# Kernel tuning notes

Hardware: AMD Instinct MI355X
Metric: run time of the kernel (lower is better)

The kernel has to match this reference:

```python
import jax, jax.numpy as jnp
import numpy as np

# Grouped TF->gene sparse decoder dims
T = 512       # number of TFs (tf_size)
K = 4         # nodes_per_tf (width_multiplier); decoder_features = T*K = 2048
G = 20000     # number of genes (gene_size)
EPG = 3       # regulating TFs per gene (TF-gene edges per gene)
B = 512       # batch of cells


def setup_inputs() -> dict:
    key = jax.random.key(0)
    k0, k1, k2, k3, k4, k5, k6 = jax.random.split(key, 7)
    features = jax.random.normal(k0, (B, T), dtype=jnp.float32)
    # Layer 1: each TF fans out to its own K hidden nodes (one weight per edge)
    w1 = jax.random.normal(k1, (T, K), dtype=jnp.float32) * 0.5
    b1 = jax.random.normal(k2, (T, K), dtype=jnp.float32) * 0.1
    # Layer 2: block-dense KxK mixing within each TF group
    w2 = jax.random.normal(k3, (T, K, K), dtype=jnp.float32) * (1.0 / np.sqrt(K))
    b2 = jax.random.normal(k4, (T, K), dtype=jnp.float32) * 0.1
    # Output layer: gene g sums over its EPG TF edges x K hidden nodes
    w3 = jax.random.normal(k5, (G, EPG, K), dtype=jnp.float32) * (1.0 / np.sqrt(EPG * K))
    b3 = jax.random.normal(k6, (G,), dtype=jnp.float32) * 0.1
    # Fixed irregular TF-gene connectivity (constant structure, like data_obj)
    edge_tf = jnp.asarray(
        np.random.default_rng(0).integers(0, T, size=(G, EPG)), dtype=jnp.int32
    )
    return {"features": features, "w1": w1, "b1": b1, "w2": w2, "b2": b2,
            "w3": w3, "b3": b3, "edge_tf": edge_tf}


def reference(features, w1, b1, w2, b2, w3, b3, edge_tf):
    # SparseLinear decoder_1: TF t -> its K hidden nodes, then LeakyReLU(0.01)
    h1 = jax.nn.leaky_relu(features[:, :, None] * w1 + b1)            # [B,T,K]
    # SparseLinear decoder_2: block-dense within each TF group + LeakyReLU
    h2 = jax.nn.leaky_relu(jnp.einsum('btj,tjk->btk', h1, w2) + b2)   # [B,T,K]
    # SparseLinear output: gather each gene's regulating TF groups, contract
    gathered = h2[:, edge_tf, :]                                      # [B,G,EPG,K]
    out = jnp.einsum('bgek,gek->bg', gathered, w3) + b3               # [B,G]
    return out
```

## Files before the change

kernel.cpp:

```cpp
#include <hip/hip_runtime.h>

namespace {

constexpr int T = 512;
constexpr int K = 4;
constexpr int G = 20000;
constexpr int EPG = 3;
constexpr int B = 512;
constexpr float SLOPE = 0.01f;

__device__ __forceinline__ float lrelu(float x) { return x > 0.0f ? x : SLOPE * x; }

__global__ __launch_bounds__(256) void h2_kernel(
    const float* __restrict__ features, const float* __restrict__ w1,
    const float* __restrict__ b1, const float* __restrict__ w2,
    const float* __restrict__ b2, float* __restrict__ h2out) {
  const int t = blockIdx.x * 256 + threadIdx.x;
  const int b = blockIdx.y;
  const float f = features[b * T + t];
  const float4 W1 = reinterpret_cast<const float4*>(w1)[t];
  const float4 B1 = reinterpret_cast<const float4*>(b1)[t];
  const float4 B2 = reinterpret_cast<const float4*>(b2)[t];
  const float h0 = lrelu(f * W1.x + B1.x);
  const float h1 = lrelu(f * W1.y + B1.y);
  const float h2 = lrelu(f * W1.z + B1.z);
  const float h3 = lrelu(f * W1.w + B1.w);
  const float4* W2 = reinterpret_cast<const float4*>(w2 + (size_t)t * (K * K));
  const float4 r0 = W2[0];
  const float4 r1 = W2[1];
  const float4 r2 = W2[2];
  const float4 r3 = W2[3];
  float4 o;
  o.x = lrelu(B2.x + h0 * r0.x + h1 * r1.x + h2 * r2.x + h3 * r3.x);
  o.y = lrelu(B2.y + h0 * r0.y + h1 * r1.y + h2 * r2.y + h3 * r3.y);
  o.z = lrelu(B2.z + h0 * r0.z + h1 * r1.z + h2 * r2.z + h3 * r3.z);
  o.w = lrelu(B2.w + h0 * r0.w + h1 * r1.w + h2 * r2.w + h3 * r3.w);
  reinterpret_cast<float4*>(h2out)[b * T + t] = o;
}

constexpr int GPT = 4;
constexpr int BTILE = 16;

__global__ __launch_bounds__(256) void out_kernel(
    const float* __restrict__ h2, const float* __restrict__ w3,
    const float* __restrict__ b3, const int* __restrict__ edge,
    float* __restrict__ out) {
  __shared__ float4 row[2][T];
  const int tid = threadIdx.x;
  const int gbase = blockIdx.x * (GPT * 256);
  const int b0 = blockIdx.y * BTILE;

  int gg[GPT];
  int te[GPT][EPG];
  float4 w3v[GPT][EPG];
  float bias[GPT];
  bool valid[GPT];
#pragma unroll
  for (int i = 0; i < GPT; ++i) {
    const int g = gbase + i * 256 + tid;
    gg[i] = g;
    valid[i] = (g < G);
    if (valid[i]) {
#pragma unroll
      for (int e = 0; e < EPG; ++e) te[i][e] = edge[g * EPG + e];
      const float4* wp = reinterpret_cast<const float4*>(w3 + (size_t)g * (EPG * K));
      w3v[i][0] = wp[0];
      w3v[i][1] = wp[1];
      w3v[i][2] = wp[2];
      bias[i] = b3[g];
    } else {
#pragma unroll
      for (int e = 0; e < EPG; ++e) te[i][e] = 0;
      w3v[i][0] = w3v[i][1] = w3v[i][2] = make_float4(0.f, 0.f, 0.f, 0.f);
      bias[i] = 0.f;
    }
  }

  {
    const float4* src = reinterpret_cast<const float4*>(h2 + (size_t)b0 * T * K);
    row[0][tid] = src[tid];
    row[0][tid + 256] = src[tid + 256];
  }

  for (int ib = 0; ib < BTILE; ++ib) {
    const int cur = ib & 1;
    __syncthreads();
    if (ib + 1 < BTILE) {
      const float4* src =
          reinterpret_cast<const float4*>(h2 + (size_t)(b0 + ib + 1) * T * K);
      row[cur ^ 1][tid] = src[tid];
      row[cur ^ 1][tid + 256] = src[tid + 256];
    }
    const int b = b0 + ib;
#pragma unroll
    for (int i = 0; i < GPT; ++i) {
      if (!valid[i]) continue;
      float acc = bias[i];
#pragma unroll
      for (int e = 0; e < EPG; ++e) {
        const float4 v = row[cur][te[i][e]];
        const float4 w = w3v[i][e];
        acc += v.x * w.x + v.y * w.y + v.z * w.z + v.w * w.w;
      }
      out[(size_t)b * G + gg[i]] = acc;
    }
  }
}

}

extern "C" void kernel_launch(void* const* d_in, const int* in_sizes, int n_in,
                              void* d_out, int out_size, void* d_ws, size_t ws_size,
                              hipStream_t stream) {
  const float* features = (const float*)d_in[0];
  const float* w1 = (const float*)d_in[1];
  const float* b1 = (const float*)d_in[2];
  const float* w2 = (const float*)d_in[3];
  const float* b2 = (const float*)d_in[4];
  const float* w3 = (const float*)d_in[5];
  const float* b3 = (const float*)d_in[6];
  const int* edge = (const int*)d_in[7];
  float* out = (float*)d_out;
  float* h2buf = (float*)d_ws;

  dim3 g1(T / 256, B);
  h2_kernel<<<g1, 256, 0, stream>>>(features, w1, b1, w2, b2, h2buf);

  dim3 g2((G + GPT * 256 - 1) / (GPT * 256), B / BTILE);
  out_kernel<<<g2, 256, 0, stream>>>(h2buf, w3, b3, edge, out);
}
```

Before: 101.4 us.

## Pack per-gene weights into records and transpose h2 tile in LDS by batch

Adds a prep kernel that packs each gene's w3 weights, bias and pre-scaled LDS byte offsets for its TFs into a 64-byte record. The output kernel loads an 8-batch tile of h2 into LDS transposed as [T][8 batches x K] with padded stride, so 8 lanes read adjacent batches of the same TF. It loops over genes with software-prefetched records. This is meant to cut per-thread register state and improve gather locality, at the cost of an extra kernel launch and rereading records for every batch tile. Output stores become strided across batches within a wave.

```diff
diff --git a/kernel.cpp b/kernel.cpp
--- a/kernel.cpp
+++ b/kernel.cpp
@@ -7,6 +7,9 @@
 constexpr int G = 20000;
 constexpr int EPG = 3;
 constexpr int B = 512;
+constexpr int GPAD = 20480;
+constexpr int ROWSTRIDE = 36;
+constexpr size_t H2_BYTES = (size_t)B * T * K * 4;
 constexpr float SLOPE = 0.01f;
 
 __device__ __forceinline__ float lrelu(float x) { return x > 0.0f ? x : SLOPE * x; }
@@ -38,72 +41,74 @@
   reinterpret_cast<float4*>(h2out)[b * T + t] = o;
 }
 
-constexpr int GPT = 4;
-constexpr int BTILE = 16;
+__global__ __launch_bounds__(256) void prep_kernel(
+    const float* __restrict__ w3, const float* __restrict__ b3,
+    const int* __restrict__ edge, float4* __restrict__ rec) {
+  const int g = blockIdx.x * 256 + threadIdx.x;
+  float4 a = make_float4(0.f, 0.f, 0.f, 0.f), b = a, c = a, d = a;
+  if (g < G) {
+    const float4* wp = reinterpret_cast<const float4*>(w3 + (size_t)g * (EPG * K));
+    a = wp[0];
+    b = wp[1];
+    c = wp[2];
+    d.x = b3[g];
+    d.y = __int_as_float(ROWSTRIDE * 4 * edge[g * EPG + 0]);
+    d.z = __int_as_float(ROWSTRIDE * 4 * edge[g * EPG + 1]);
+    d.w = __int_as_float(ROWSTRIDE * 4 * edge[g * EPG + 2]);
+  } else {
+    d.y = d.z = d.w = __int_as_float(0);
+  }
+  float4* o = rec + (size_t)g * 4;
+  o[0] = a; o[1] = b; o[2] = c; o[3] = d;
+}
 
-__global__ __launch_bounds__(256) void out_kernel(
-    const float* __restrict__ h2, const float* __restrict__ w3,
-    const float* __restrict__ b3, const int* __restrict__ edge,
+__global__ __launch_bounds__(256) void out_kernel_v2(
+    const float* __restrict__ h2, const float4* __restrict__ rec,
     float* __restrict__ out) {
-  __shared__ float4 row[2][T];
+  extern __shared__ float lds[];
   const int tid = threadIdx.x;
-  const int gbase = blockIdx.x * (GPT * 256);
-  const int b0 = blockIdx.y * BTILE;
+  const int gbase = blockIdx.x * 1024;
+  const int b0 = blockIdx.y * 8;
 
-  int gg[GPT];
-  int te[GPT][EPG];
-  float4 w3v[GPT][EPG];
-  float bias[GPT];
-  bool valid[GPT];
+  {
+    const float4* src = reinterpret_cast<const float4*>(h2 + (size_t)b0 * (T * K));
 #pragma unroll
-  for (int i = 0; i < GPT; ++i) {
-    const int g = gbase + i * 256 + tid;
-    gg[i] = g;
-    valid[i] = (g < G);
-    if (valid[i]) {
-#pragma unroll
-      for (int e = 0; e < EPG; ++e) te[i][e] = edge[g * EPG + e];
-      const float4* wp = reinterpret_cast<const float4*>(w3 + (size_t)g * (EPG * K));
-      w3v[i][0] = wp[0];
-      w3v[i][1] = wp[1];
-      w3v[i][2] = wp[2];
-      bias[i] = b3[g];
-    } else {
-#pragma unroll
-      for (int e = 0; e < EPG; ++e) te[i][e] = 0;
-      w3v[i][0] = w3v[i][1] = w3v[i][2] = make_float4(0.f, 0.f, 0.f, 0.f);
-      bias[i] = 0.f;
+    for (int j = 0; j < 16; ++j) {
+      const int f = j * 256 + tid;
+      const int bb = f >> 9;
+      const int t = f & 511;
+      const float4 v = src[(size_t)bb * T + t];
+      *reinterpret_cast<float4*>(lds + ROWSTRIDE * t + 4 * bb) = v;
     }
   }
+  __syncthreads();
 
+  const int bidx = tid & 7;
+  const int gsub = tid >> 3;
+  const char* ldsb = reinterpret_cast<const char*>(lds);
+  const int laneoff = bidx * 16;
+
+  float4 p0, p1, p2, p3;
   {
-    const float4* src = reinterpret_cast<const float4*>(h2 + (size_t)b0 * T * K);
-    row[0][tid] = src[tid];
-    row[0][tid + 256] = src[tid + 256];
+    const float4* r = rec + (size_t)(gbase + gsub) * 4;
+    p0 = r[0]; p1 = r[1]; p2 = r[2]; p3 = r[3];
   }
-
-  for (int ib = 0; ib < BTILE; ++ib) {
-    const int cur = ib & 1;
-    __syncthreads();
-    if (ib + 1 < BTILE) {
-      const float4* src =
-          reinterpret_cast<const float4*>(h2 + (size_t)(b0 + ib + 1) * T * K);
-      row[cur ^ 1][tid] = src[tid];
-      row[cur ^ 1][tid + 256] = src[tid + 256];
+#pragma unroll 4
+  for (int s = 0; s < 32; ++s) {
+    const float4 c0 = p0, c1 = p1, c2 = p2, c3 = p3;
+    const int g = gbase + s * 32 + gsub;
+    if (s + 1 < 32) {
+      const float4* r = rec + (size_t)(gbase + (s + 1) * 32 + gsub) * 4;
+      p0 = r[0]; p1 = r[1]; p2 = r[2]; p3 = r[3];
     }
-    const int b = b0 + ib;
-#pragma unroll
-    for (int i = 0; i < GPT; ++i) {
-      if (!valid[i]) continue;
-      float acc = bias[i];
-#pragma unroll
-      for (int e = 0; e < EPG; ++e) {
-        const float4 v = row[cur][te[i][e]];
-        const float4 w = w3v[i][e];
-        acc += v.x * w.x + v.y * w.y + v.z * w.z + v.w * w.w;
-      }
-      out[(size_t)b * G + gg[i]] = acc;
-    }
+    const float4 v0 = *reinterpret_cast<const float4*>(ldsb + (__float_as_int(c3.y) + laneoff));
+    const float4 v1 = *reinterpret_cast<const float4*>(ldsb + (__float_as_int(c3.z) + laneoff));
+    const float4 v2 = *reinterpret_cast<const float4*>(ldsb + (__float_as_int(c3.w) + laneoff));
+    float acc = c3.x;
+    acc += v0.x * c0.x + v0.y * c0.y + v0.z * c0.z + v0.w * c0.w;
+    acc += v1.x * c1.x + v1.y * c1.y + v1.z * c1.z + v1.w * c1.w;
+    acc += v2.x * c2.x + v2.y * c2.y + v2.z * c2.z + v2.w * c2.w;
+    if (g < G) out[(size_t)(b0 + bidx) * G + g] = acc;
   }
 }
 
@@ -121,11 +126,22 @@
   const float* b3 = (const float*)d_in[6];
   const int* edge = (const int*)d_in[7];
   float* out = (float*)d_out;
+
   float* h2buf = (float*)d_ws;
+  float4* rec = (float4*)((char*)d_ws + H2_BYTES);
 
   dim3 g1(T / 256, B);
   h2_kernel<<<g1, 256, 0, stream>>>(features, w1, b1, w2, b2, h2buf);
 
-  dim3 g2((G + GPT * 256 - 1) / (GPT * 256), B / BTILE);
-  out_kernel<<<g2, 256, 0, stream>>>(h2buf, w3, b3, edge, out);
+  prep_kernel<<<GPAD / 256, 256, 0, stream>>>(w3, b3, edge, rec);
+
+  static bool attr_set = false;
+  if (!attr_set) {
+    hipFuncSetAttribute((const void*)out_kernel_v2,
+                        hipFuncAttributeMaxDynamicSharedMemorySize,
+                        T * ROWSTRIDE * 4);
+    attr_set = true;
+  }
+  dim3 g2(GPAD / 1024, B / 8);
+  out_kernel_v2<<<g2, 256, T * ROWSTRIDE * 4, stream>>>(h2buf, rec, out);
 }
```

Result: slower. 124.1 us (+22.4%).

## Transpose h2 to TF-major layout and gather per-batch-thread with packed gene records

Applied to the files above, without the earlier changes.

Stores h2 TF-major as [T][B] float4 so each thread owns one batch row and gathers a gene's three TF vectors with coalesced loads across the wavefront. A prep kernel packs each gene's weights, bias and pre-scaled edge byte offsets into one 64-byte record. The output kernel handles 16 genes by 256 batch rows per block and transposes the results through padded LDS so global writes stay coalesced. This drops the per-block shared-memory row staging and its barriers, at the cost of an extra kernel launch and an extra pass over w3 each call.

```diff
diff --git a/kernel.cpp b/kernel.cpp
--- a/kernel.cpp
+++ b/kernel.cpp
@@ -7,17 +7,21 @@
 constexpr int G = 20000;
 constexpr int EPG = 3;
 constexpr int B = 512;
+constexpr int GC = 16;
+constexpr int NGB = G / GC;
+constexpr int LPAD = 20;
 constexpr float SLOPE = 0.01f;
+constexpr size_t H2T_OFF = 2u << 20;
 
 __device__ __forceinline__ float lrelu(float x) { return x > 0.0f ? x : SLOPE * x; }
 
-__global__ __launch_bounds__(256) void h2_kernel(
+__global__ __launch_bounds__(256) void h2t_kernel(
     const float* __restrict__ features, const float* __restrict__ w1,
     const float* __restrict__ b1, const float* __restrict__ w2,
-    const float* __restrict__ b2, float* __restrict__ h2out) {
-  const int t = blockIdx.x * 256 + threadIdx.x;
-  const int b = blockIdx.y;
-  const float f = features[b * T + t];
+    const float* __restrict__ b2, float* __restrict__ h2t) {
+  const int t = blockIdx.x;
+  const int b = blockIdx.y * 256 + threadIdx.x;
+  const float f = features[(size_t)b * T + t];
   const float4 W1 = reinterpret_cast<const float4*>(w1)[t];
   const float4 B1 = reinterpret_cast<const float4*>(b1)[t];
   const float4 B2 = reinterpret_cast<const float4*>(b2)[t];
@@ -35,75 +39,61 @@
   o.y = lrelu(B2.y + h0 * r0.y + h1 * r1.y + h2 * r2.y + h3 * r3.y);
   o.z = lrelu(B2.z + h0 * r0.z + h1 * r1.z + h2 * r2.z + h3 * r3.z);
   o.w = lrelu(B2.w + h0 * r0.w + h1 * r1.w + h2 * r2.w + h3 * r3.w);
-  reinterpret_cast<float4*>(h2out)[b * T + t] = o;
+  reinterpret_cast<float4*>(h2t)[(size_t)t * B + b] = o;
 }
 
-constexpr int GPT = 4;
-constexpr int BTILE = 16;
+__global__ __launch_bounds__(256) void prep_kernel(
+    const float* __restrict__ w3, const float* __restrict__ b3,
+    const int* __restrict__ edge, float4* __restrict__ rec) {
+  const int g = blockIdx.x * 256 + threadIdx.x;
+  if (g >= G) return;
+  const float4* wp = reinterpret_cast<const float4*>(w3 + (size_t)g * (EPG * K));
+  const float4 a = wp[0], b = wp[1], c = wp[2];
+  float4 d;
+  d.x = b3[g];
+  d.y = __int_as_float(edge[g * EPG + 0] * (B * K * 4));
+  d.z = __int_as_float(edge[g * EPG + 1] * (B * K * 4));
+  d.w = __int_as_float(edge[g * EPG + 2] * (B * K * 4));
+  float4* o = rec + (size_t)g * 4;
+  o[0] = a; o[1] = b; o[2] = c; o[3] = d;
+}
 
-__global__ __launch_bounds__(256) void out_kernel(
-    const float* __restrict__ h2, const float* __restrict__ w3,
-    const float* __restrict__ b3, const int* __restrict__ edge,
+__global__ __launch_bounds__(256) void out_kernel_v3(
+    const float* __restrict__ h2t, const float4* __restrict__ rec,
     float* __restrict__ out) {
-  __shared__ float4 row[2][T];
+  __shared__ float lds[256 * LPAD];
   const int tid = threadIdx.x;
-  const int gbase = blockIdx.x * (GPT * 256);
-  const int b0 = blockIdx.y * BTILE;
-
-  int gg[GPT];
-  int te[GPT][EPG];
-  float4 w3v[GPT][EPG];
-  float bias[GPT];
-  bool valid[GPT];
+  const int g0 = blockIdx.x * GC;
+  const char* h2b = reinterpret_cast<const char*>(h2t) +
+                    ((size_t)blockIdx.y * 256 + tid) * 16;
+  float acc[GC];
 #pragma unroll
-  for (int i = 0; i < GPT; ++i) {
-    const int g = gbase + i * 256 + tid;
-    gg[i] = g;
-    valid[i] = (g < G);
-    if (valid[i]) {
+  for (int gi = 0; gi < GC; ++gi) {
+    const float4* r = rec + (size_t)(g0 + gi) * 4;
+    const float4 w0 = r[0];
+    const float4 w1v = r[1];
+    const float4 w2v = r[2];
+    const float4 m = r[3];
+    const float4 v0 = *reinterpret_cast<const float4*>(h2b + __float_as_int(m.y));
+    const float4 v1 = *reinterpret_cast<const float4*>(h2b + __float_as_int(m.z));
+    const float4 v2 = *reinterpret_cast<const float4*>(h2b + __float_as_int(m.w));
+    float a = m.x;
+    a += v0.x * w0.x + v0.y * w0.y + v0.z * w0.z + v0.w * w0.w;
+    a += v1.x * w1v.x + v1.y * w1v.y + v1.z * w1v.z + v1.w * w1v.w;
+    a += v2.x * w2v.x + v2.y * w2v.y + v2.z * w2v.z + v2.w * w2v.w;
+    acc[gi] = a;
+  }
 #pragma unroll
-      for (int e = 0; e < EPG; ++e) te[i][e] = edge[g * EPG + e];
-      const float4* wp = reinterpret_cast<const float4*>(w3 + (size_t)g * (EPG * K));
-      w3v[i][0] = wp[0];
-      w3v[i][1] = wp[1];
-      w3v[i][2] = wp[2];
-      bias[i] = b3[g];
-    } else {
+  for (int q = 0; q < GC / 4; ++q)
+    *reinterpret_cast<float4*>(&lds[tid * LPAD + q * 4]) =
+        make_float4(acc[q * 4 + 0], acc[q * 4 + 1], acc[q * 4 + 2], acc[q * 4 + 3]);
+  __syncthreads();
 #pragma unroll
-      for (int e = 0; e < EPG; ++e) te[i][e] = 0;
-      w3v[i][0] = w3v[i][1] = w3v[i][2] = make_float4(0.f, 0.f, 0.f, 0.f);
-      bias[i] = 0.f;
-    }
-  }
-
-  {
-    const float4* src = reinterpret_cast<const float4*>(h2 + (size_t)b0 * T * K);
-    row[0][tid] = src[tid];
-    row[0][tid + 256] = src[tid + 256];
-  }
-
-  for (int ib = 0; ib < BTILE; ++ib) {
-    const int cur = ib & 1;
-    __syncthreads();
-    if (ib + 1 < BTILE) {
-      const float4* src =
-          reinterpret_cast<const float4*>(h2 + (size_t)(b0 + ib + 1) * T * K);
-      row[cur ^ 1][tid] = src[tid];
-      row[cur ^ 1][tid + 256] = src[tid + 256];
-    }
-    const int b = b0 + ib;
-#pragma unroll
-    for (int i = 0; i < GPT; ++i) {
-      if (!valid[i]) continue;
-      float acc = bias[i];
-#pragma unroll
-      for (int e = 0; e < EPG; ++e) {
-        const float4 v = row[cur][te[i][e]];
-        const float4 w = w3v[i][e];
-        acc += v.x * w.x + v.y * w.y + v.z * w.z + v.w * w.w;
-      }
-      out[(size_t)b * G + gg[i]] = acc;
-    }
+  for (int j = 0; j < GC; ++j) {
+    const int flat = j * 256 + tid;
+    const int brow = flat >> 4;
+    const int gcol = flat & 15;
+    out[((size_t)blockIdx.y * 256 + brow) * G + g0 + gcol] = lds[brow * LPAD + gcol];
   }
 }
 
@@ -121,11 +111,15 @@
   const float* b3 = (const float*)d_in[6];
   const int* edge = (const int*)d_in[7];
   float* out = (float*)d_out;
-  float* h2buf = (float*)d_ws;
 
-  dim3 g1(T / 256, B);
-  h2_kernel<<<g1, 256, 0, stream>>>(features, w1, b1, w2, b2, h2buf);
+  float4* rec = (float4*)d_ws;
+  float* h2t = (float*)((char*)d_ws + H2T_OFF);
 
-  dim3 g2((G + GPT * 256 - 1) / (GPT * 256), B / BTILE);
-  out_kernel<<<g2, 256, 0, stream>>>(h2buf, w3, b3, edge, out);
+  dim3 g1(T, B / 256);
+  h2t_kernel<<<g1, 256, 0, stream>>>(features, w1, b1, w2, b2, h2t);
+
+  prep_kernel<<<(G + 255) / 256, 256, 0, stream>>>(w3, b3, edge, rec);
+
+  dim3 g2(NGB, B / 256);
+  out_kernel_v3<<<g2, 256, 0, stream>>>(h2t, rec, out);
 }
```

After: 107.6 us. 6.1% more time.
